# Performance work log

Measured on AMD Instinct MI355X. Metric: run time of the kernel, lower is better.

The kernel has to match this reference:

```python
import jax, jax.numpy as jnp
import numpy as np

L, D, H, DFF = 12, 768, 12, 3072
DH = D // H
EPS = 1e-5


def _layer_norm(x, g, b):
    # manual LN as in source: biased variance, eps inside sqrt
    mean = jnp.mean(x, axis=-1, keepdims=True)
    var = jnp.mean((x - mean) ** 2, axis=-1, keepdims=True)
    return g * (x - mean) / jnp.sqrt(var + EPS) + b


def setup_inputs() -> dict:
    key = jax.random.key(0)
    ks = jax.random.split(key, 10)
    x = jax.random.normal(ks[0], (8, 512, D), dtype=jnp.float32)
    mask = jnp.zeros((8, 1, 1, 512), dtype=jnp.float32)
    s = 0.02
    Wq = jax.random.normal(ks[1], (L, D, D), jnp.float32) * s
    Wk = jax.random.normal(ks[2], (L, D, D), jnp.float32) * s
    Wv = jax.random.normal(ks[3], (L, D, D), jnp.float32) * s
    Wo = jax.random.normal(ks[4], (L, D, D), jnp.float32) * s
    W1 = jax.random.normal(ks[5], (L, DFF, D), jnp.float32) * s
    W2 = jax.random.normal(ks[6], (L, D, DFF), jnp.float32) * s
    z = lambda *sh: jnp.zeros(sh, jnp.float32)
    o = lambda *sh: jnp.ones(sh, jnp.float32)
    return {
        'x': x, 'mask': mask,
        'Wq': Wq, 'bq': z(L, D), 'Wk': Wk, 'bk': z(L, D), 'Wv': Wv, 'bv': z(L, D),
        'Wo': Wo, 'bo': z(L, D), 'g1': o(L, D), 'b1': z(L, D),
        'W1': W1, 'bf1': z(L, DFF), 'W2': W2, 'bf2': z(L, D),
        'g2': o(L, D), 'b2': z(L, D),
    }


def reference(x, mask, Wq, bq, Wk, bk, Wv, bv, Wo, bo, g1, b1, W1, bf1, W2, bf2, g2, b2):
    B, S, _ = x.shape
    scale = 1.0 / jnp.sqrt(jnp.float32(DH))

    def layer(h, p):
        wq, pq, wk, pk, wv, pv, wo, po, gg1, bb1, w1, pf1, w2, pf2, gg2, bb2 = p
        # Dense: x @ W^T + b
        q = (h @ wq.T + pq).reshape(B, S, H, DH).transpose(0, 2, 1, 3)  # [B,H,S,dh]
        k = (h @ wk.T + pk).reshape(B, S, H, DH).transpose(0, 2, 1, 3)
        v = (h @ wv.T + pv).reshape(B, S, H, DH).transpose(0, 2, 1, 3)
        scores = jnp.einsum('bhqd,bhkd->bhqk', q, k) * scale
        scores = scores + mask * -1e9
        attn = jax.nn.softmax(scores, axis=-1)
        ctx = jnp.einsum('bhqk,bhkd->bhqd', attn, v)
        ctx = ctx.transpose(0, 2, 1, 3).reshape(B, S, D)
        a = _layer_norm(h + (ctx @ wo.T + po), gg1, bb1)
        ffn = jnp.maximum(a @ w1.T + pf1, 0.0) @ w2.T + pf2
        out = _layer_norm(a + ffn, gg2, bb2)
        return out, None

    params = (Wq, bq, Wk, bk, Wv, bv, Wo, bo, g1, b1, W1, bf1, W2, bf2, g2, b2)
    out, _ = jax.lax.scan(layer, x, params)
    return out
```

## Files before the change

kernel.cpp:

```cpp
#include <hip/hip_runtime.h>
#include <hip/hip_bf16.h>
#include <stdint.h>

#define DDIM 768
#define NH 12
#define DHD 64
#define DFF 3072
#define NLAYER 12
#define SEQ 512
#define NB 8
#define ROWS (NB*SEQ)

typedef __attribute__((ext_vector_type(4))) float f32x4;
typedef __attribute__((ext_vector_type(8))) short short8;

static __device__ __forceinline__ short bf16r(float f) {
  union { float f; uint32_t u; } a; a.f = f;
  uint32_t u = a.u;
  u += 0x7FFFu + ((u >> 16) & 1u);
  return (short)(u >> 16);
}

static __device__ __forceinline__ float bf2f(short s) {
  union { uint32_t u; float f; } c;
  c.u = ((uint32_t)(uint16_t)s) << 16;
  return c.f;
}

static __device__ __forceinline__ f32x4 mfma_bf16(short8 a, short8 b, f32x4 c) {
  return __builtin_amdgcn_mfma_f32_16x16x32_bf16(a, b, c, 0, 0, 0);
}

static __device__ __forceinline__ void gload16(const void* g, void* l) {
  __builtin_amdgcn_global_load_lds(
      (__attribute__((address_space(1))) void*)(void*)(uintptr_t)g,
      (__attribute__((address_space(3))) void*)l,
      16, 0, 0);
}

struct WCvt {
  const float* src[4];
  short* dst[4];
  int n8[4];
};

__global__ void wconv_kernel(WCvt wc) {
  const int m = blockIdx.y;
  const float* __restrict__ src = wc.src[m];
  short* __restrict__ dst = wc.dst[m];
  const int n8 = wc.n8[m];
  for (int i = blockIdx.x * 256 + threadIdx.x; i < n8; i += gridDim.x * 256) {
    f32x4 a = *(const f32x4*)(src + (size_t)i * 8);
    f32x4 b = *(const f32x4*)(src + (size_t)i * 8 + 4);
    short8 o;
    o[0] = bf16r(a[0]); o[1] = bf16r(a[1]); o[2] = bf16r(a[2]); o[3] = bf16r(a[3]);
    o[4] = bf16r(b[0]); o[5] = bf16r(b[1]); o[6] = bf16r(b[2]); o[7] = bf16r(b[3]);
    *(short8*)(dst + (size_t)i * 8) = o;
  }
}

struct GemmB {
  const short* W0; const short* W1; const short* W2;
  const float* b0; const float* b1; const float* b2;
  void* o0; void* o1; void* o2;
};

template<int OUTMODE, int BM>
__launch_bounds__(256, 2)
__global__ void gemm_bt(const short* __restrict__ A, GemmB gb, int M, int N, int K) {
  constexpr int MF  = BM / 32;
  constexpr int ISS = BM / 64;

  const int z = blockIdx.z;
  const short* W    = (z == 0) ? gb.W0 : ((z == 1) ? gb.W1 : gb.W2);
  const float* bias = (z == 0) ? gb.b0 : ((z == 1) ? gb.b1 : gb.b2);
  void* outp        = (z == 0) ? gb.o0 : ((z == 1) ? gb.o1 : gb.o2);

  __shared__ __align__(16) short As[2][BM * 32];
  __shared__ __align__(16) short Bs[2][128 * 32];

  const int tid  = threadIdx.x;
  const int lane = tid & 63;
  const int wid  = tid >> 6;
  const int l16  = lane & 15;
  const int kg   = lane >> 4;
  const int wr   = wid >> 1;
  const int wc   = wid & 1;
  const int m0   = blockIdx.x * BM;
  const int n0   = blockIdx.y * 128;

  const f32x4 zero = {0.f, 0.f, 0.f, 0.f};
  f32x4 acc[MF][4];
  #pragma unroll
  for (int i = 0; i < MF; i++)
    #pragma unroll
    for (int j = 0; j < 4; j++) acc[i][j] = zero;

  const int lrow = lane >> 2;
  const int lcol = (lane & 3) * 8;
  const short* Ag = A + (size_t)(m0 + wid * (BM / 4) + lrow) * K + lcol;
  const short* Wg = W + (size_t)(n0 + wid * 32 + lrow) * K + lcol;

  auto stage = [&](int buf, int k0) {
    #pragma unroll
    for (int j = 0; j < ISS; j++)
      gload16(Ag + k0 + (size_t)(j * 16) * K, &As[buf][(wid * (BM / 4) + j * 16) * 32]);
    #pragma unroll
    for (int j = 0; j < 2; j++)
      gload16(Wg + k0 + (size_t)(j * 16) * K, &Bs[buf][(wid * 32 + j * 16) * 32]);
  };

  auto compute = [&](int buf) {
    short8 af[MF], bfr[4];
    #pragma unroll
    for (int i = 0; i < MF; i++)
      af[i] = *(const short8*)&As[buf][(wr * (BM / 2) + i * 16 + l16) * 32 + kg * 8];
    #pragma unroll
    for (int j = 0; j < 4; j++)
      bfr[j] = *(const short8*)&Bs[buf][(wc * 64 + j * 16 + l16) * 32 + kg * 8];
    #pragma unroll
    for (int i = 0; i < MF; i++)
      #pragma unroll
      for (int j = 0; j < 4; j++)
        acc[i][j] = mfma_bf16(af[i], bfr[j], acc[i][j]);
  };

  const int nsteps = K >> 5;
  stage(0, 0);
  __syncthreads();
  for (int s = 0; s < nsteps; s += 2) {
    stage(1, (s + 1) << 5);
    compute(0);
    __syncthreads();
    if (s + 2 < nsteps) stage(0, (s + 2) << 5);
    compute(1);
    __syncthreads();
  }

  float* outf = (float*)outp;
  short* outb = (short*)outp;
  #pragma unroll
  for (int j = 0; j < 4; j++) {
    const int col = n0 + wc * 64 + j * 16 + l16;
    const float bv = bias[col];
    #pragma unroll
    for (int i = 0; i < MF; i++) {
      const int row0 = m0 + wr * (BM / 2) + i * 16 + kg * 4;
      #pragma unroll
      for (int e = 0; e < 4; e++) {
        float v = acc[i][j][e] + bv;
        if (OUTMODE == 2) v = fmaxf(v, 0.0f);
        const size_t off = (size_t)(row0 + e) * N + col;
        if (OUTMODE == 0) outf[off] = v;
        else              outb[off] = bf16r(v);
      }
    }
  }
}

__launch_bounds__(256, 2)
__global__ void attn_kernel(const short* __restrict__ Qg, const short* __restrict__ Kg,
                            const short* __restrict__ Vg, const float* __restrict__ mask,
                            short* __restrict__ ctx) {
  __shared__ __align__(16) short Vt[64 * 512];

  const int bh = blockIdx.x;
  const int b = bh / NH;
  const int h = bh % NH;
  const int tid  = threadIdx.x;
  const int lane = tid & 63;
  const int wid  = tid >> 6;
  const int l16  = lane & 15;
  const int kg   = lane >> 4;

  const short* Qb = Qg + (size_t)b * SEQ * DDIM + h * DHD;
  const short* Kb = Kg + (size_t)b * SEQ * DDIM + h * DHD;
  const short* Vb = Vg + (size_t)b * SEQ * DDIM + h * DHD;

  for (int c = tid; c < SEQ * 8; c += 256) {
    const int kv = c >> 3;
    const int d0 = (c & 7) * 8;
    short8 v = *(const short8*)(Vb + (size_t)kv * DDIM + d0);
    #pragma unroll
    for (int j = 0; j < 8; j++)
      Vt[(d0 + j) * 512 + (kv ^ ((j & 3) << 3))] = v[j];
  }
  __syncthreads();

  const int q0 = blockIdx.y * 128 + wid * 32;

  short8 qf[2][2];
  #pragma unroll
  for (int rt = 0; rt < 2; rt++)
    #pragma unroll
    for (int dh = 0; dh < 2; dh++)
      qf[rt][dh] = *(const short8*)(Qb + (size_t)(q0 + rt * 16 + l16) * DDIM + dh * 32 + kg * 8);

  float mrun[2] = {-1e30f, -1e30f};
  float lrun[2] = {0.0f, 0.0f};
  const f32x4 zero = {0.f, 0.f, 0.f, 0.f};
  f32x4 oacc[2][4];
  #pragma unroll
  for (int rt = 0; rt < 2; rt++)
    #pragma unroll
    for (int dt = 0; dt < 4; dt++) oacc[rt][dt] = zero;

  const float* maskb = mask + (size_t)b * SEQ;

  for (int kv0 = 0; kv0 < SEQ; kv0 += 32) {
    short8 kf[2][2];
    #pragma unroll
    for (int kvh = 0; kvh < 2; kvh++)
      #pragma unroll
      for (int dh = 0; dh < 2; dh++)
        kf[kvh][dh] = *(const short8*)(Kb + (size_t)(kv0 + kvh * 16 + l16) * DDIM + dh * 32 + kg * 8);

    short8 vf[4];
    #pragma unroll
    for (int dt = 0; dt < 4; dt++) {
      const int d = dt * 16 + l16;
      vf[dt] = *(const short8*)&Vt[d * 512 + ((kv0 + kg * 8) ^ ((d & 3) << 3))];
    }

    const f32x4 mq0 = *(const f32x4*)(maskb + kv0 + kg * 4);
    const f32x4 mq1 = *(const f32x4*)(maskb + kv0 + 16 + kg * 4);

    #pragma unroll
    for (int rt = 0; rt < 2; rt++) {
      f32x4 s0 = zero, s1 = zero;
      s0 = mfma_bf16(kf[0][0], qf[rt][0], s0);
      s0 = mfma_bf16(kf[0][1], qf[rt][1], s0);
      s1 = mfma_bf16(kf[1][0], qf[rt][0], s1);
      s1 = mfma_bf16(kf[1][1], qf[rt][1], s1);

      float p[8];
      #pragma unroll
      for (int e = 0; e < 4; e++) {
        p[e]     = s0[e] * 0.125f + mq0[e] * (-1e9f);
        p[e + 4] = s1[e] * 0.125f + mq1[e] * (-1e9f);
      }
      float mt = p[0];
      #pragma unroll
      for (int e = 1; e < 8; e++) mt = fmaxf(mt, p[e]);
      mt = fmaxf(mt, __shfl_xor(mt, 16, 64));
      mt = fmaxf(mt, __shfl_xor(mt, 32, 64));
      const float mnew = fmaxf(mrun[rt], mt);
      const float corr = __expf(mrun[rt] - mnew);
      float ts = 0.0f;
      #pragma unroll
      for (int e = 0; e < 8; e++) { p[e] = __expf(p[e] - mnew); ts += p[e]; }
      ts += __shfl_xor(ts, 16, 64);
      ts += __shfl_xor(ts, 32, 64);
      lrun[rt] = lrun[rt] * corr + ts;
      mrun[rt] = mnew;

      const int P0 = (int)(((uint32_t)(uint16_t)bf16r(p[1]) << 16) | (uint16_t)bf16r(p[0]));
      const int P1 = (int)(((uint32_t)(uint16_t)bf16r(p[3]) << 16) | (uint16_t)bf16r(p[2]));
      const int P2 = (int)(((uint32_t)(uint16_t)bf16r(p[5]) << 16) | (uint16_t)bf16r(p[4]));
      const int P3 = (int)(((uint32_t)(uint16_t)bf16r(p[7]) << 16) | (uint16_t)bf16r(p[6]));
      const int sl0 = (((2 * kg) & 3) << 4) + l16;
      const int sl1 = (((2 * kg + 1) & 3) << 4) + l16;
      const int x0 = __shfl(P0, sl0, 64), y0 = __shfl(P2, sl0, 64);
      const int x1 = __shfl(P1, sl0, 64), y1 = __shfl(P3, sl0, 64);
      const int x2 = __shfl(P0, sl1, 64), y2 = __shfl(P2, sl1, 64);
      const int x3 = __shfl(P1, sl1, 64), y3 = __shfl(P3, sl1, 64);
      union { int w[4]; short8 v; } pa;
      const bool hi = (kg >= 2);
      pa.w[0] = hi ? y0 : x0;
      pa.w[1] = hi ? y1 : x1;
      pa.w[2] = hi ? y2 : x2;
      pa.w[3] = hi ? y3 : x3;

      const float c0 = __shfl(corr, kg * 4 + 0, 64);
      const float c1 = __shfl(corr, kg * 4 + 1, 64);
      const float c2 = __shfl(corr, kg * 4 + 2, 64);
      const float c3 = __shfl(corr, kg * 4 + 3, 64);

      #pragma unroll
      for (int dt = 0; dt < 4; dt++) {
        f32x4 o = oacc[rt][dt];
        o[0] *= c0; o[1] *= c1; o[2] *= c2; o[3] *= c3;
        oacc[rt][dt] = mfma_bf16(pa.v, vf[dt], o);
      }
    }
  }

  short* cb = ctx + (size_t)b * SEQ * DDIM + h * DHD;
  #pragma unroll
  for (int rt = 0; rt < 2; rt++) {
    const float li = 1.0f / lrun[rt];
    const float l0 = __shfl(li, kg * 4 + 0, 64);
    const float l1 = __shfl(li, kg * 4 + 1, 64);
    const float l2 = __shfl(li, kg * 4 + 2, 64);
    const float l3 = __shfl(li, kg * 4 + 3, 64);
    #pragma unroll
    for (int dt = 0; dt < 4; dt++) {
      const f32x4 o = oacc[rt][dt];
      const int col = dt * 16 + l16;
      const size_t base = (size_t)(q0 + rt * 16 + kg * 4) * DDIM + col;
      cb[base + 0 * DDIM] = bf16r(o[0] * l0);
      cb[base + 1 * DDIM] = bf16r(o[1] * l1);
      cb[base + 2 * DDIM] = bf16r(o[2] * l2);
      cb[base + 3 * DDIM] = bf16r(o[3] * l3);
    }
  }
}

template<int PBF16>
__launch_bounds__(256, 4)
__global__ void ln_kernel(const float* __restrict__ resid, const void* __restrict__ projv,
                          const float* __restrict__ gw, const float* __restrict__ bw,
                          float* __restrict__ outf, short* __restrict__ outb) {
  const int lane = threadIdx.x & 63;
  const int wid  = threadIdx.x >> 6;
  const int row  = blockIdx.x * 4 + wid;
  const float* rp = resid + (size_t)row * DDIM;
  float v[12];
  float s = 0.0f;
  #pragma unroll
  for (int c = 0; c < 12; c++) {
    float pv;
    if (PBF16) pv = bf2f(((const short*)projv)[(size_t)row * DDIM + c * 64 + lane]);
    else       pv = ((const float*)projv)[(size_t)row * DDIM + c * 64 + lane];
    v[c] = rp[c * 64 + lane] + pv;
    s += v[c];
  }
  #pragma unroll
  for (int o = 1; o < 64; o <<= 1) s += __shfl_xor(s, o, 64);
  const float mean = s * (1.0f / 768.0f);
  float q = 0.0f;
  #pragma unroll
  for (int c = 0; c < 12; c++) { const float d = v[c] - mean; q += d * d; }
  #pragma unroll
  for (int o = 1; o < 64; o <<= 1) q += __shfl_xor(q, o, 64);
  const float inv = 1.0f / sqrtf(q * (1.0f / 768.0f) + 1e-5f);
  #pragma unroll
  for (int c = 0; c < 12; c++) {
    const int idx = c * 64 + lane;
    const float y = gw[idx] * (v[c] - mean) * inv + bw[idx];
    outf[(size_t)row * DDIM + idx] = y;
    outb[(size_t)row * DDIM + idx] = bf16r(y);
  }
}

extern "C" void kernel_launch(void* const* d_in, const int* in_sizes, int n_in,
                              void* d_out, int out_size, void* d_ws, size_t ws_size,
                              hipStream_t stream) {
  const float* x    = (const float*)d_in[0];
  const float* mask = (const float*)d_in[1];
  const float* Wq   = (const float*)d_in[2];
  const float* bq   = (const float*)d_in[3];
  const float* Wk   = (const float*)d_in[4];
  const float* bk   = (const float*)d_in[5];
  const float* Wv   = (const float*)d_in[6];
  const float* bv   = (const float*)d_in[7];
  const float* Wo   = (const float*)d_in[8];
  const float* bo   = (const float*)d_in[9];
  const float* g1   = (const float*)d_in[10];
  const float* b1   = (const float*)d_in[11];
  const float* W1   = (const float*)d_in[12];
  const float* bf1  = (const float*)d_in[13];
  const float* W2   = (const float*)d_in[14];
  const float* bf2  = (const float*)d_in[15];
  const float* g2   = (const float*)d_in[16];
  const float* b2   = (const float*)d_in[17];

  const size_t SD  = (size_t)ROWS * DDIM;
  const size_t WDD = (size_t)DDIM * DDIM;
  const size_t WFD = (size_t)DFF * DDIM;

  char* ws = (char*)d_ws;
  float* H0   = (float*)ws;  ws += SD * 4;
  short* Bbuf = (short*)ws;  ws += SD * 2;
  short* R1   = (short*)ws;  ws += (size_t)ROWS * DFF * 2;
  short* WB   = (short*)ws;

  short* Qb = R1;
  short* Kb = R1 + SD;
  short* Vb = R1 + 2 * SD;
  short* Cb = R1 + 3 * SD;
  float* Pf = (float*)R1;

  {
    WCvt c{};
    c.src[0] = x; c.dst[0] = Bbuf; c.n8[0] = (int)(SD / 8);
    wconv_kernel<<<dim3(1536, 1), 256, 0, stream>>>(c);
  }

  for (int l = 0; l < NLAYER; l++) {
    {
      WCvt c{};
      c.src[0] = Wq + l * WDD; c.dst[0] = WB;           c.n8[0] = (int)(WDD / 8);
      c.src[1] = Wk + l * WDD; c.dst[1] = WB + WDD;     c.n8[1] = (int)(WDD / 8);
      c.src[2] = Wv + l * WDD; c.dst[2] = WB + 2 * WDD; c.n8[2] = (int)(WDD / 8);
      c.src[3] = Wo + l * WDD; c.dst[3] = WB + 3 * WDD; c.n8[3] = (int)(WDD / 8);
      wconv_kernel<<<dim3(288, 4), 256, 0, stream>>>(c);
    }

    {
      GemmB g{};
      g.W0 = WB;           g.b0 = bq + l * DDIM; g.o0 = Qb;
      g.W1 = WB + WDD;     g.b1 = bk + l * DDIM; g.o1 = Kb;
      g.W2 = WB + 2 * WDD; g.b2 = bv + l * DDIM; g.o2 = Vb;
      gemm_bt<1, 128><<<dim3(32, 6, 3), 256, 0, stream>>>(Bbuf, g, ROWS, DDIM, DDIM);
    }

    attn_kernel<<<dim3(NB * NH, 4), 256, 0, stream>>>(Qb, Kb, Vb, mask, Cb);

    {
      GemmB g{};
      g.W0 = WB + 3 * WDD; g.b0 = bo + l * DDIM; g.o0 = Pf;
      gemm_bt<0, 64><<<dim3(64, 6, 1), 256, 0, stream>>>(Cb, g, ROWS, DDIM, DDIM);
    }

    {
      WCvt c{};
      c.src[0] = W1 + l * WFD; c.dst[0] = WB;       c.n8[0] = (int)(WFD / 8);
      c.src[1] = W2 + l * WFD; c.dst[1] = WB + WFD; c.n8[1] = (int)(WFD / 8);
      wconv_kernel<<<dim3(1152, 2), 256, 0, stream>>>(c);
    }

    ln_kernel<0><<<dim3(ROWS / 4), 256, 0, stream>>>(l ? H0 : x, Pf,
                                                     g1 + l * DDIM, b1 + l * DDIM,
                                                     H0, Bbuf);

    {
      GemmB g{};
      g.W0 = WB; g.b0 = bf1 + l * DFF; g.o0 = R1;
      gemm_bt<2, 128><<<dim3(32, 24, 1), 256, 0, stream>>>(Bbuf, g, ROWS, DFF, DDIM);
    }

    {
      GemmB g{};
      g.W0 = WB + WFD; g.b0 = bf2 + l * DDIM; g.o0 = Bbuf;
      gemm_bt<1, 64><<<dim3(64, 6, 1), 256, 0, stream>>>(R1, g, ROWS, DDIM, DFF);
    }

    ln_kernel<1><<<dim3(ROWS / 4), 256, 0, stream>>>(H0, Bbuf,
                                                     g2 + l * DDIM, b2 + l * DDIM,
                                                     (l == NLAYER - 1) ? (float*)d_out : H0,
                                                     Bbuf);
  }
}
```

Baseline: 2.265 ms.

## Restructure GEMM main loop into two-stage prefetch pipeline with explicit waitcnt barriers

Rewrites the GEMM K-loop so two LDS stages are kept in flight. Each iteration reads its fragments, waits only on LDS, barriers, then issues the global-to-LDS prefetch for step t+2 before the MFMAs. Partial vmcnt waits replace full __syncthreads drains, and launch bounds go from 2 to 3 blocks per CU to raise occupancy. The hand-counted vmcnt values depend on how gload16 is lowered, and the tighter register budget risks spilling.

```diff
diff --git a/kernel.cpp b/kernel.cpp
--- a/kernel.cpp
+++ b/kernel.cpp
@@ -13,6 +13,12 @@
 
 typedef __attribute__((ext_vector_type(4))) float f32x4;
 typedef __attribute__((ext_vector_type(8))) short short8;
+
+#define S_BARRIER()  asm volatile("s_barrier" ::: "memory")
+#define WAIT_LGKM0() asm volatile("s_waitcnt lgkmcnt(0)" ::: "memory")
+#define WAIT_VM0()   asm volatile("s_waitcnt vmcnt(0)" ::: "memory")
+#define WAIT_VM3()   asm volatile("s_waitcnt vmcnt(3)" ::: "memory")
+#define WAIT_VM4()   asm volatile("s_waitcnt vmcnt(4)" ::: "memory")
 
 static __device__ __forceinline__ short bf16r(float f) {
   union { float f; uint32_t u; } a; a.f = f;
@@ -66,7 +72,7 @@
 };
 
 template<int OUTMODE, int BM>
-__launch_bounds__(256, 2)
+__launch_bounds__(256, 3)
 __global__ void gemm_bt(const short* __restrict__ A, GemmB gb, int M, int N, int K) {
   constexpr int MF  = BM / 32;
   constexpr int ISS = BM / 64;
@@ -110,31 +116,37 @@
       gload16(Wg + k0 + (size_t)(j * 16) * K, &Bs[buf][(wid * 32 + j * 16) * 32]);
   };
 
-  auto compute = [&](int buf) {
+  const int nsteps = K >> 5;
+  stage(0, 0);
+  stage(1, 32);
+  if (ISS == 2) { WAIT_VM4(); } else { WAIT_VM3(); }
+  S_BARRIER();
+
+  for (int t = 0; t < nsteps; ++t) {
+    const int cur = t & 1;
     short8 af[MF], bfr[4];
     #pragma unroll
     for (int i = 0; i < MF; i++)
-      af[i] = *(const short8*)&As[buf][(wr * (BM / 2) + i * 16 + l16) * 32 + kg * 8];
+      af[i] = *(const short8*)&As[cur][(wr * (BM / 2) + i * 16 + l16) * 32 + kg * 8];
     #pragma unroll
     for (int j = 0; j < 4; j++)
-      bfr[j] = *(const short8*)&Bs[buf][(wc * 64 + j * 16 + l16) * 32 + kg * 8];
+      bfr[j] = *(const short8*)&Bs[cur][(wc * 64 + j * 16 + l16) * 32 + kg * 8];
+    WAIT_LGKM0();
+    S_BARRIER();
+
+    const bool pf = (t + 2 < nsteps);
+    if (pf) stage(cur, (t + 2) << 5);
+    __builtin_amdgcn_sched_barrier(0);
     #pragma unroll
     for (int i = 0; i < MF; i++)
       #pragma unroll
       for (int j = 0; j < 4; j++)
         acc[i][j] = mfma_bf16(af[i], bfr[j], acc[i][j]);
-  };
-
-  const int nsteps = K >> 5;
-  stage(0, 0);
-  __syncthreads();
-  for (int s = 0; s < nsteps; s += 2) {
-    stage(1, (s + 1) << 5);
-    compute(0);
-    __syncthreads();
-    if (s + 2 < nsteps) stage(0, (s + 2) << 5);
-    compute(1);
-    __syncthreads();
+    __builtin_amdgcn_sched_barrier(0);
+
+    if (pf) { if (ISS == 2) { WAIT_VM4(); } else { WAIT_VM3(); } }
+    else    { WAIT_VM0(); }
+    S_BARRIER();
   }
 
   float* outf = (float*)outp;
```

Measured after the change: 2.099 ms, median of 2. 7.3% less time.
